# Kernel optimization log

Measured on AMD Instinct MI355X. Metric: run time of the kernel, lower is better.

## Reference

```python
import jax, jax.numpy as jnp
import numpy as np

N, K, DC, DH = 50000, 32, 64, 64  # nodes, neighbors, dim_c(+dim_h), dim_hidden

def setup_inputs() -> dict:
    key = jax.random.key(0)
    ks = jax.random.split(key, 8)
    return {
        "z":     jax.random.normal(ks[0], (N, DC), dtype=jnp.float32),
        "z_":    jax.random.normal(ks[1], (N, K, DC), dtype=jnp.float32),
        "W_cur": jax.random.normal(ks[2], (DC, DH), dtype=jnp.float32) * 0.1,
        "b_cur": jax.random.uniform(ks[3], (DH,), minval=-0.1, maxval=0.1, dtype=jnp.float32),
        "W_nbr": jax.random.normal(ks[4], (2 * DC, DH), dtype=jnp.float32) * 0.1,
        "b_nbr": jax.random.uniform(ks[5], (DH,), minval=-0.1, maxval=0.1, dtype=jnp.float32),
        "W_out": jax.random.normal(ks[6], (2 * DH, DC), dtype=jnp.float32) * 0.1,
        "b_out": jax.random.uniform(ks[7], (DC,), minval=-0.1, maxval=0.1, dtype=jnp.float32),
    }

def reference(z, z_, W_cur, b_cur, W_nbr, b_nbr, W_out, b_out):
    # cur branch: CELU(Linear(z))  -> [N, DH]
    v = jax.nn.celu(z @ W_cur + b_cur)
    # nbr branch: concat(self expanded over nbr axis, neighbors) -> [N, K, 2*DC]
    zz = jnp.concatenate((jnp.broadcast_to(z[:, None, :], z_.shape), z_), axis=-1)
    # CELU(Linear) then sum over neighbor axis -> [N, DH]
    v_ = jax.nn.celu(zz @ W_nbr + b_nbr).sum(axis=-2)
    # final linear on concatenated features -> [N, DC]
    dc = jnp.concatenate((v, v_), axis=-1) @ W_out + b_out
    return dc
```

## Files before the change

kernel.cpp:

```cpp
#include <hip/hip_runtime.h>
#include <hip/hip_bf16.h>

typedef float  f32x16 __attribute__((ext_vector_type(16)));
typedef short  bf16x8 __attribute__((ext_vector_type(8)));

__device__ __forceinline__ unsigned short f2bf(float x) {
  union { float f; unsigned u; } v; v.f = x;
  return (unsigned short)((v.u + 0x7FFFu + ((v.u >> 16) & 1u)) >> 16);
}
__device__ __forceinline__ float bf2f(unsigned short u) {
  union { unsigned u; float f; } v; v.u = ((unsigned)u) << 16; return v.f;
}
__device__ __forceinline__ float celu1(float x) {
  return x > 0.f ? x : (__expf(x) - 1.f);
}

__device__ __forceinline__ bf16x8 to_frag(float4 a, float4 b) {
  bf16x8 r;
  r[0] = (short)f2bf(a.x); r[1] = (short)f2bf(a.y);
  r[2] = (short)f2bf(a.z); r[3] = (short)f2bf(a.w);
  r[4] = (short)f2bf(b.x); r[5] = (short)f2bf(b.y);
  r[6] = (short)f2bf(b.z); r[7] = (short)f2bf(b.w);
  return r;
}

__device__ __forceinline__ bf16x8 ldsfrag(const unsigned short* w, int S, int col, int k0) {
  return *reinterpret_cast<const bf16x8*>(w + col * S + (k0 ^ ((col & 7) << 3)));
}

__device__ __forceinline__ bf16x8 wfrag(const float* __restrict__ W, int ld, int col, int k0) {
  bf16x8 f;
#pragma unroll
  for (int j = 0; j < 8; ++j) f[j] = (short)f2bf(W[(size_t)(k0 + j) * ld + col]);
  return f;
}

__global__ __launch_bounds__(256, 2) void gcu_kernel(
    const float* __restrict__ z, const float* __restrict__ z_,
    const float* __restrict__ Wc, const float* __restrict__ bc,
    const float* __restrict__ Wn, const float* __restrict__ bn,
    const float* __restrict__ Wo, const float* __restrict__ bo,
    float* __restrict__ out, int N) {
  __shared__ __align__(16) unsigned short sWnT[64 * 128];
  __shared__ __align__(16) unsigned short sT[4][32 * 64];
  __shared__ __align__(16) unsigned short sV[4][32 * 64];
  __shared__ __align__(16) float sTile[4][32 * 64];

  const int tid = threadIdx.x;
  const int wid = tid >> 6, lane = tid & 63;
  const int lo = lane & 31, hi = lane >> 5;

  for (int i = tid; i < 128 * 64; i += 256) {
    int c = i & 63, k = i >> 6;
    sWnT[c * 128 + (k ^ ((c & 7) << 3))] = f2bf(Wn[i]);
  }
  __syncthreads();

  const int gw = blockIdx.x * 4 + wid;
  const int nwaves = (int)gridDim.x * 4;
  const int start = (int)((long long)gw * N / nwaves);
  const int end   = (int)((long long)(gw + 1) * N / nwaves);
  const int cnt = end - start;
  if (cnt <= 0) return;

  unsigned short* tt = &sT[wid][0];
  unsigned short* sv = &sV[wid][0];
  float* tile = &sTile[wid][0];

  const int rl = lane >> 4, tl = lane & 15;
  const int o0 = rl * 64 + ((tl ^ rl) << 2);
  const int o1 = o0 ^ 16;

  auto stage_tile = [&](const float* gb) {
#pragma unroll
    for (int i = 0; i < 8; ++i) {
      const float* src = gb + i * 256 + ((i & 1) ? o1 : o0);
      __builtin_amdgcn_global_load_lds(
          (const __attribute__((address_space(1))) unsigned*)src,
          (__attribute__((address_space(3))) unsigned*)(tile + i * 256),
          16, 0, 0);
    }
  };

  stage_tile(z_ + (size_t)start * 2048);

  const float bn0 = bn[lo], bn1 = bn[32 + lo];
  const float bc0 = bc[lo], bc1 = bc[32 + lo];
  const float bo0 = bo[lo], bo1 = bo[32 + lo];

  bf16x8 zf[4];
  {
    int node = min(start + lo, N - 1);
    const float* zp = z + (size_t)node * 64;
#pragma unroll
    for (int ks = 0; ks < 4; ++ks) {
      float4 x0 = *reinterpret_cast<const float4*>(zp + ks * 16 + 8 * hi);
      float4 x1 = *reinterpret_cast<const float4*>(zp + ks * 16 + 8 * hi + 4);
      zf[ks] = to_frag(x0, x1);
    }
  }

  {
    f32x16 a0{}, a1{};
#pragma unroll
    for (int ks = 0; ks < 4; ++ks) {
      int k0 = ks * 16 + 8 * hi;
      bf16x8 b0 = ldsfrag(sWnT, 128, lo, k0);
      bf16x8 b1 = ldsfrag(sWnT, 128, lo + 32, k0);
      a0 = __builtin_amdgcn_mfma_f32_32x32x16_bf16(zf[ks], b0, a0, 0, 0, 0);
      a1 = __builtin_amdgcn_mfma_f32_32x32x16_bf16(zf[ks], b1, a1, 0, 0, 0);
    }
#pragma unroll
    for (int r = 0; r < 16; ++r) {
      int row = (r & 3) + 8 * (r >> 2) + 4 * hi;
      tt[row * 64 + lo]      = f2bf(a0[r]);
      tt[row * 64 + 32 + lo] = f2bf(a1[r]);
    }
  }

  bf16x8 Bn_[4][2];
#pragma unroll
  for (int ks = 0; ks < 4; ++ks) {
    int k0 = 64 + ks * 16 + 8 * hi;
    Bn_[ks][0] = ldsfrag(sWnT, 128, lo, k0);
    Bn_[ks][1] = ldsfrag(sWnT, 128, lo + 32, k0);
  }

  int roff[8];
#pragma unroll
  for (int ks = 0; ks < 4; ++ks)
#pragma unroll
    for (int p = 0; p < 2; ++p)
      roff[ks * 2 + p] = lo * 256 + (((ks * 4 + 2 * hi + p) ^ (lo & 7)) << 4);
  const char* tb = (const char*)tile;

#pragma unroll 1
  for (int nn = 0; nn < cnt; ++nn) {
    asm volatile("s_waitcnt vmcnt(0)" ::: "memory");
    __builtin_amdgcn_sched_barrier(0);
    float4 q[8];
#pragma unroll
    for (int j = 0; j < 8; ++j) q[j] = *reinterpret_cast<const float4*>(tb + roff[j]);
    bf16x8 af[4];
#pragma unroll
    for (int ks = 0; ks < 4; ++ks) af[ks] = to_frag(q[2 * ks], q[2 * ks + 1]);
    asm volatile("s_waitcnt lgkmcnt(0)" ::: "memory");
    __builtin_amdgcn_sched_barrier(0);
    if (nn + 1 < cnt) stage_tile(z_ + (size_t)(start + nn + 1) * 2048);

    float c0 = bn0 + bf2f(tt[nn * 64 + lo]);
    float c1 = bn1 + bf2f(tt[nn * 64 + 32 + lo]);
    f32x16 acc0{}, acc1{};
#pragma unroll
    for (int ks = 0; ks < 4; ++ks) {
      acc0 = __builtin_amdgcn_mfma_f32_32x32x16_bf16(af[ks], Bn_[ks][0], acc0, 0, 0, 0);
      acc1 = __builtin_amdgcn_mfma_f32_32x32x16_bf16(af[ks], Bn_[ks][1], acc1, 0, 0, 0);
    }
    float s0 = 0.f, s1 = 0.f;
#pragma unroll
    for (int r = 0; r < 16; ++r) {
      s0 += celu1(acc0[r] + c0);
      s1 += celu1(acc1[r] + c1);
    }
    s0 += __shfl_xor(s0, 32, 64);
    s1 += __shfl_xor(s1, 32, 64);
    if (hi == 0) {
      int m = (nn & 7) << 3;
      sv[nn * 64 + ( lo       ^ m)] = f2bf(s0);
      sv[nn * 64 + ((32 + lo) ^ m)] = f2bf(s1);
    }
  }

  unsigned short* vt = (unsigned short*)tile;
  asm volatile("s_waitcnt vmcnt(0)" ::: "memory");
  {
    f32x16 a0{}, a1{};
#pragma unroll
    for (int ks = 0; ks < 4; ++ks) {
      int k0 = ks * 16 + 8 * hi;
      a0 = __builtin_amdgcn_mfma_f32_32x32x16_bf16(zf[ks], wfrag(Wc, 64, lo, k0), a0, 0, 0, 0);
      a1 = __builtin_amdgcn_mfma_f32_32x32x16_bf16(zf[ks], wfrag(Wc, 64, lo + 32, k0), a1, 0, 0, 0);
    }
#pragma unroll
    for (int r = 0; r < 16; ++r) {
      int row = (r & 3) + 8 * (r >> 2) + 4 * hi;
      int m = (row & 7) << 3;
      vt[row * 64 + ( lo       ^ m)] = f2bf(celu1(a0[r] + bc0));
      vt[row * 64 + ((32 + lo) ^ m)] = f2bf(celu1(a1[r] + bc1));
    }
  }

  {
    f32x16 a0{}, a1{};
    const int mm = (lo & 7) << 3;
#pragma unroll
    for (int ks = 0; ks < 8; ++ks) {
      int k0 = ks * 16 + 8 * hi;
      bf16x8 af;
      if (ks < 4) af = *reinterpret_cast<const bf16x8*>(vt + lo * 64 + ( k0        ^ mm));
      else        af = *reinterpret_cast<const bf16x8*>(sv + lo * 64 + ((k0 - 64)  ^ mm));
      a0 = __builtin_amdgcn_mfma_f32_32x32x16_bf16(af, wfrag(Wo, 64, lo, k0), a0, 0, 0, 0);
      a1 = __builtin_amdgcn_mfma_f32_32x32x16_bf16(af, wfrag(Wo, 64, lo + 32, k0), a1, 0, 0, 0);
    }
#pragma unroll
    for (int r = 0; r < 16; ++r) {
      int row = start + (r & 3) + 8 * (r >> 2) + 4 * hi;
      if (row < end) {
        out[(size_t)row * 64 + lo]      = a0[r] + bo0;
        out[(size_t)row * 64 + 32 + lo] = a1[r] + bo1;
      }
    }
  }
}

extern "C" void kernel_launch(void* const* d_in, const int* in_sizes, int n_in,
                              void* d_out, int out_size, void* d_ws, size_t ws_size,
                              hipStream_t stream) {
  const float* z  = (const float*)d_in[0];
  const float* z_ = (const float*)d_in[1];
  const float* Wc = (const float*)d_in[2];
  const float* bc = (const float*)d_in[3];
  const float* Wn = (const float*)d_in[4];
  const float* bn = (const float*)d_in[5];
  const float* Wo = (const float*)d_in[6];
  const float* bo = (const float*)d_in[7];
  float* out = (float*)d_out;
  const int N = in_sizes[0] / 64;
  gcu_kernel<<<512, 256, 0, stream>>>(z, z_, Wc, bc, Wn, bn, Wo, bo, out, N);
}
```

Baseline: 92.27 us.

## Split neighbor tile staging into two halves for finer-grained load/compute overlap

Each node's 32x64 neighbor tile is now staged as two halves of four 16-byte global-to-LDS loads. The loop waits only on vmcnt(4) per half, so the next node's half-tile is in flight while the current half feeds the MFMAs. The LDS layout changes from a swizzled row layout to a column-chunk layout that matches the MFMA A-fragment directly, which drops the per-lane offset table. MFMA sections get raised wave priority via s_setprio. The last iteration now prefetches a clamped, redundant tile instead of skipping it, which adds some extra traffic and risks LDS bank conflicts from the unswizzled layout.

After: 95.25 us. 1.03x slower.

```diff
diff --git a/kernel.cpp b/kernel.cpp
--- a/kernel.cpp
+++ b/kernel.cpp
@@ -67,22 +67,17 @@
   unsigned short* sv = &sV[wid][0];
   float* tile = &sTile[wid][0];
 
-  const int rl = lane >> 4, tl = lane & 15;
-  const int o0 = rl * 64 + ((tl ^ rl) << 2);
-  const int o1 = o0 ^ 16;
-
-  auto stage_tile = [&](const float* gb) {
-#pragma unroll
-    for (int i = 0; i < 8; ++i) {
-      const float* src = gb + i * 256 + ((i & 1) ? o1 : o0);
+  const int srcoff = (lane & 31) * 64 + (lane >> 5) * 4;
+  auto stage4 = [&](const float* gb, int h) {
+#pragma unroll
+    for (int c = 0; c < 4; ++c) {
+      const float* src = gb + srcoff + (4 * h + c) * 8;
       __builtin_amdgcn_global_load_lds(
           (const __attribute__((address_space(1))) unsigned*)src,
-          (__attribute__((address_space(3))) unsigned*)(tile + i * 256),
+          (__attribute__((address_space(3))) unsigned*)(tile + (4 * h + c) * 256),
           16, 0, 0);
     }
   };
-
-  stage_tile(z_ + (size_t)start * 2048);
 
   const float bn0 = bn[lo], bn1 = bn[32 + lo];
   const float bc0 = bc[lo], bc1 = bc[32 + lo];
@@ -99,6 +94,10 @@
       zf[ks] = to_frag(x0, x1);
     }
   }
+  __builtin_amdgcn_sched_barrier(0);
+
+  stage4(z_ + (size_t)start * 2048, 0);
+  stage4(z_ + (size_t)start * 2048, 1);
 
   {
     f32x16 a0{}, a1{};
@@ -126,36 +125,33 @@
     Bn_[ks][1] = ldsfrag(sWnT, 128, lo + 32, k0);
   }
 
-  int roff[8];
-#pragma unroll
-  for (int ks = 0; ks < 4; ++ks)
-#pragma unroll
-    for (int p = 0; p < 2; ++p)
-      roff[ks * 2 + p] = lo * 256 + (((ks * 4 + 2 * hi + p) ^ (lo & 7)) << 4);
-  const char* tb = (const char*)tile;
+  const char* tbyte = (const char*)tile;
 
 #pragma unroll 1
   for (int nn = 0; nn < cnt; ++nn) {
-    asm volatile("s_waitcnt vmcnt(0)" ::: "memory");
-    __builtin_amdgcn_sched_barrier(0);
-    float4 q[8];
-#pragma unroll
-    for (int j = 0; j < 8; ++j) q[j] = *reinterpret_cast<const float4*>(tb + roff[j]);
-    bf16x8 af[4];
-#pragma unroll
-    for (int ks = 0; ks < 4; ++ks) af[ks] = to_frag(q[2 * ks], q[2 * ks + 1]);
-    asm volatile("s_waitcnt lgkmcnt(0)" ::: "memory");
-    __builtin_amdgcn_sched_barrier(0);
-    if (nn + 1 < cnt) stage_tile(z_ + (size_t)(start + nn + 1) * 2048);
-
+    const float* nxt = z_ + (size_t)min(start + nn + 1, N - 1) * 2048;
+    f32x16 acc0{}, acc1{};
+#pragma unroll
+    for (int h = 0; h < 2; ++h) {
+      asm volatile("s_waitcnt vmcnt(4)" ::: "memory");
+      __builtin_amdgcn_sched_barrier(0);
+      float4 q0 = *reinterpret_cast<const float4*>(tbyte + (4 * h + hi) * 1024 + lo * 16);
+      float4 q1 = *reinterpret_cast<const float4*>(tbyte + (4 * h + hi) * 1024 + 512 + lo * 16);
+      float4 q2 = *reinterpret_cast<const float4*>(tbyte + (4 * h + 2 + hi) * 1024 + lo * 16);
+      float4 q3 = *reinterpret_cast<const float4*>(tbyte + (4 * h + 2 + hi) * 1024 + 512 + lo * 16);
+      asm volatile("s_waitcnt lgkmcnt(0)" ::: "memory");
+      __builtin_amdgcn_sched_barrier(0);
+      stage4(nxt, h);
+      bf16x8 af0 = to_frag(q0, q1), af1 = to_frag(q2, q3);
+      __builtin_amdgcn_s_setprio(1);
+      acc0 = __builtin_amdgcn_mfma_f32_32x32x16_bf16(af0, Bn_[2 * h][0],     acc0, 0, 0, 0);
+      acc1 = __builtin_amdgcn_mfma_f32_32x32x16_bf16(af0, Bn_[2 * h][1],     acc1, 0, 0, 0);
+      acc0 = __builtin_amdgcn_mfma_f32_32x32x16_bf16(af1, Bn_[2 * h + 1][0], acc0, 0, 0, 0);
+      acc1 = __builtin_amdgcn_mfma_f32_32x32x16_bf16(af1, Bn_[2 * h + 1][1], acc1, 0, 0, 0);
+      __builtin_amdgcn_s_setprio(0);
+    }
     float c0 = bn0 + bf2f(tt[nn * 64 + lo]);
     float c1 = bn1 + bf2f(tt[nn * 64 + 32 + lo]);
-    f32x16 acc0{}, acc1{};
-#pragma unroll
-    for (int ks = 0; ks < 4; ++ks) {
-      acc0 = __builtin_amdgcn_mfma_f32_32x32x16_bf16(af[ks], Bn_[ks][0], acc0, 0, 0, 0);
-      acc1 = __builtin_amdgcn_mfma_f32_32x32x16_bf16(af[ks], Bn_[ks][1], acc1, 0, 0, 0);
-    }
     float s0 = 0.f, s1 = 0.f;
 #pragma unroll
     for (int r = 0; r < 16; ++r) {
@@ -171,8 +167,10 @@
     }
   }
 
+  asm volatile("s_waitcnt vmcnt(0)" ::: "memory");
+  __builtin_amdgcn_sched_barrier(0);
+
   unsigned short* vt = (unsigned short*)tile;
-  asm volatile("s_waitcnt vmcnt(0)" ::: "memory");
   {
     f32x16 a0{}, a1{};
 #pragma unroll
@@ -197,8 +195,8 @@
     for (int ks = 0; ks < 8; ++ks) {
       int k0 = ks * 16 + 8 * hi;
       bf16x8 af;
-      if (ks < 4) af = *reinterpret_cast<const bf16x8*>(vt + lo * 64 + ( k0        ^ mm));
-      else        af = *reinterpret_cast<const bf16x8*>(sv + lo * 64 + ((k0 - 64)  ^ mm));
+      if (ks < 4) af = *reinterpret_cast<const bf16x8*>(vt + lo * 64 + ( k0       ^ mm));
+      else        af = *reinterpret_cast<const bf16x8*>(sv + lo * 64 + ((k0 - 64) ^ mm));
       a0 = __builtin_amdgcn_mfma_f32_32x32x16_bf16(af, wfrag(Wo, 64, lo, k0), a0, 0, 0, 0);
       a1 = __builtin_amdgcn_mfma_f32_32x32x16_bf16(af, wfrag(Wo, 64, lo + 32, k0), a1, 0, 0, 0);
     }
```

## Double-buffer neighbor tiles using alternating LDS and register staging

Applied to the files above, without the earlier changes.

Processes nodes in pairs. Even nodes stream their neighbor tile through LDS via global_load_lds, and odd nodes load theirs directly into registers, so one tile is always in flight while the other is computed. The wait counts are relaxed to vmcnt(8), so the next load no longer has to drain before compute starts. Out-of-range prefetches are clamped to N-1, which trades some extra loads and more register pressure for deeper prefetch.

Result: no change. 93.07 us (+0.9%).

```diff
diff --git a/kernel.cpp b/kernel.cpp
--- a/kernel.cpp
+++ b/kernel.cpp
@@ -34,6 +34,8 @@
   for (int j = 0; j < 8; ++j) f[j] = (short)f2bf(W[(size_t)(k0 + j) * ld + col]);
   return f;
 }
+
+struct Stage { float4 a[4][2]; };
 
 __global__ __launch_bounds__(256, 2) void gcu_kernel(
     const float* __restrict__ z, const float* __restrict__ z_,
@@ -70,7 +72,6 @@
   const int rl = lane >> 4, tl = lane & 15;
   const int o0 = rl * 64 + ((tl ^ rl) << 2);
   const int o1 = o0 ^ 16;
-
   auto stage_tile = [&](const float* gb) {
 #pragma unroll
     for (int i = 0; i < 8; ++i) {
@@ -81,8 +82,15 @@
           16, 0, 0);
     }
   };
-
-  stage_tile(z_ + (size_t)start * 2048);
+  auto issue_stage = [&](Stage& s, const float* aptr) {
+#pragma unroll
+    for (int ks = 0; ks < 4; ++ks) {
+      const float* pa = aptr + lo * 64 + ks * 16 + 8 * hi;
+      s.a[ks][0] = *reinterpret_cast<const float4*>(pa);
+      s.a[ks][1] = *reinterpret_cast<const float4*>(pa + 4);
+    }
+  };
+  auto nodep = [&](int n) { return z_ + (size_t)min(start + n, N - 1) * 2048; };
 
   const float bn0 = bn[lo], bn1 = bn[32 + lo];
   const float bc0 = bc[lo], bc1 = bc[32 + lo];
@@ -99,6 +107,11 @@
       zf[ks] = to_frag(x0, x1);
     }
   }
+  __builtin_amdgcn_sched_barrier(0);
+
+  Stage stg;
+  stage_tile(nodep(0));
+  issue_stage(stg, nodep(1));
 
   {
     f32x16 a0{}, a1{};
@@ -134,28 +147,9 @@
       roff[ks * 2 + p] = lo * 256 + (((ks * 4 + 2 * hi + p) ^ (lo & 7)) << 4);
   const char* tb = (const char*)tile;
 
-#pragma unroll 1
-  for (int nn = 0; nn < cnt; ++nn) {
-    asm volatile("s_waitcnt vmcnt(0)" ::: "memory");
-    __builtin_amdgcn_sched_barrier(0);
-    float4 q[8];
-#pragma unroll
-    for (int j = 0; j < 8; ++j) q[j] = *reinterpret_cast<const float4*>(tb + roff[j]);
-    bf16x8 af[4];
-#pragma unroll
-    for (int ks = 0; ks < 4; ++ks) af[ks] = to_frag(q[2 * ks], q[2 * ks + 1]);
-    asm volatile("s_waitcnt lgkmcnt(0)" ::: "memory");
-    __builtin_amdgcn_sched_barrier(0);
-    if (nn + 1 < cnt) stage_tile(z_ + (size_t)(start + nn + 1) * 2048);
-
+  auto finish = [&](f32x16& acc0, f32x16& acc1, int nn) {
     float c0 = bn0 + bf2f(tt[nn * 64 + lo]);
     float c1 = bn1 + bf2f(tt[nn * 64 + 32 + lo]);
-    f32x16 acc0{}, acc1{};
-#pragma unroll
-    for (int ks = 0; ks < 4; ++ks) {
-      acc0 = __builtin_amdgcn_mfma_f32_32x32x16_bf16(af[ks], Bn_[ks][0], acc0, 0, 0, 0);
-      acc1 = __builtin_amdgcn_mfma_f32_32x32x16_bf16(af[ks], Bn_[ks][1], acc1, 0, 0, 0);
-    }
     float s0 = 0.f, s1 = 0.f;
 #pragma unroll
     for (int r = 0; r < 16; ++r) {
@@ -169,10 +163,67 @@
       sv[nn * 64 + ( lo       ^ m)] = f2bf(s0);
       sv[nn * 64 + ((32 + lo) ^ m)] = f2bf(s1);
     }
-  }
+  };
+
+  const int pairs = cnt >> 1, odd = cnt & 1;
+
+#pragma unroll 1
+  for (int i = 0; i < pairs; ++i) {
+    asm volatile("s_waitcnt vmcnt(8)" ::: "memory");
+    __builtin_amdgcn_sched_barrier(0);
+    float4 q[8];
+#pragma unroll
+    for (int j = 0; j < 8; ++j) q[j] = *reinterpret_cast<const float4*>(tb + roff[j]);
+    asm volatile("s_waitcnt lgkmcnt(0)" ::: "memory");
+    __builtin_amdgcn_sched_barrier(0);
+    stage_tile(nodep(2 * i + 2));
+    {
+      f32x16 acc0{}, acc1{};
+#pragma unroll
+      for (int ks = 0; ks < 4; ++ks) {
+        bf16x8 af = to_frag(q[2 * ks], q[2 * ks + 1]);
+        acc0 = __builtin_amdgcn_mfma_f32_32x32x16_bf16(af, Bn_[ks][0], acc0, 0, 0, 0);
+        acc1 = __builtin_amdgcn_mfma_f32_32x32x16_bf16(af, Bn_[ks][1], acc1, 0, 0, 0);
+      }
+      finish(acc0, acc1, 2 * i);
+    }
+    asm volatile("s_waitcnt vmcnt(8)" ::: "memory");
+    __builtin_amdgcn_sched_barrier(0);
+    bf16x8 bf_[4];
+#pragma unroll
+    for (int ks = 0; ks < 4; ++ks) bf_[ks] = to_frag(stg.a[ks][0], stg.a[ks][1]);
+    issue_stage(stg, nodep(2 * i + 3));
+    {
+      f32x16 acc0{}, acc1{};
+#pragma unroll
+      for (int ks = 0; ks < 4; ++ks) {
+        acc0 = __builtin_amdgcn_mfma_f32_32x32x16_bf16(bf_[ks], Bn_[ks][0], acc0, 0, 0, 0);
+        acc1 = __builtin_amdgcn_mfma_f32_32x32x16_bf16(bf_[ks], Bn_[ks][1], acc1, 0, 0, 0);
+      }
+      finish(acc0, acc1, 2 * i + 1);
+    }
+  }
+
+  if (odd) {
+    asm volatile("s_waitcnt vmcnt(8)" ::: "memory");
+    __builtin_amdgcn_sched_barrier(0);
+    float4 q[8];
+#pragma unroll
+    for (int j = 0; j < 8; ++j) q[j] = *reinterpret_cast<const float4*>(tb + roff[j]);
+    f32x16 acc0{}, acc1{};
+#pragma unroll
+    for (int ks = 0; ks < 4; ++ks) {
+      bf16x8 af = to_frag(q[2 * ks], q[2 * ks + 1]);
+      acc0 = __builtin_amdgcn_mfma_f32_32x32x16_bf16(af, Bn_[ks][0], acc0, 0, 0, 0);
+      acc1 = __builtin_amdgcn_mfma_f32_32x32x16_bf16(af, Bn_[ks][1], acc1, 0, 0, 0);
+    }
+    finish(acc0, acc1, cnt - 1);
+  }
+
+  asm volatile("s_waitcnt vmcnt(0)" ::: "memory");
+  __builtin_amdgcn_sched_barrier(0);
 
   unsigned short* vt = (unsigned short*)tile;
-  asm volatile("s_waitcnt vmcnt(0)" ::: "memory");
   {
     f32x16 a0{}, a1{};
 #pragma unroll
@@ -197,8 +248,8 @@
     for (int ks = 0; ks < 8; ++ks) {
       int k0 = ks * 16 + 8 * hi;
       bf16x8 af;
-      if (ks < 4) af = *reinterpret_cast<const bf16x8*>(vt + lo * 64 + ( k0        ^ mm));
-      else        af = *reinterpret_cast<const bf16x8*>(sv + lo * 64 + ((k0 - 64)  ^ mm));
+      if (ks < 4) af = *reinterpret_cast<const bf16x8*>(vt + lo * 64 + ( k0       ^ mm));
+      else        af = *reinterpret_cast<const bf16x8*>(sv + lo * 64 + ((k0 - 64) ^ mm));
       a0 = __builtin_amdgcn_mfma_f32_32x32x16_bf16(af, wfrag(Wo, 64, lo, k0), a0, 0, 0, 0);
       a1 = __builtin_amdgcn_mfma_f32_32x32x16_bf16(af, wfrag(Wo, 64, lo + 32, k0), a1, 0, 0, 0);
     }
```
